# Optimization experiments

Hardware: AMD Instinct MI355X
Metric: run time of the kernel (lower is better)

The kernel has to match this reference:

```python
import jax, jax.numpy as jnp
import numpy as np
from jax import lax

# Production-scale dims: batch, seq_len, tag_size (incl. START/STOP tags)
B, S, T = 512, 512, 64


def setup_inputs() -> dict:
    key = jax.random.key(0)
    k1, k2, k3, k4 = jax.random.split(key, 4)
    feats = jax.random.normal(k1, (B, S, T), dtype=jnp.float32)
    # prefix-contiguous mask (module assumes mask[:, 0] == 1 and length-style masks)
    lengths = jax.random.randint(k2, (B,), S // 2, S + 1)
    mask = jnp.arange(S)[None, :] < lengths[:, None]  # (B, S) bool
    tags = jax.random.randint(k3, (B, S), 0, T - 2)  # gold tags exclude START/STOP
    transitions = jax.random.normal(k4, (T, T), dtype=jnp.float32) * 0.1
    return {"feats": feats, "mask": mask, "tags": tags, "transitions": transitions}


def _crf_nll(feats, transitions, mask, tags):
    b, s, t = feats.shape
    START, STOP = t - 2, t - 1  # START_TAG = -2, STOP_TAG = -1

    # ---- forward (log partition), matches _calculate_PZ ----
    # partition init: scores[0][:, START, :] = feats[:,0,:] + transitions[START, :]
    init = feats[:, 0, :] + transitions[START][None, :]  # (b, t)

    feats_t = jnp.swapaxes(feats, 0, 1)  # (s, b, t)
    mask_t = jnp.swapaxes(mask, 0, 1)    # (s, b)

    def step(partition, inp):
        f_t, m_t = inp  # (b, t), (b,)
        # cur_values[b, from, to] = feats_t[b, to] + transitions[from, to] + partition[b, from]
        cur = partition[:, :, None] + transitions[None, :, :] + f_t[:, None, :]
        new_p = jax.nn.logsumexp(cur, axis=1)  # reduce over 'from' -> (b, t)
        partition = jnp.where(m_t[:, None], new_p, partition)
        return partition, None

    partition, _ = lax.scan(step, init, (feats_t[1:], mask_t[1:]))

    # final transition to STOP
    final = jax.nn.logsumexp(partition[:, :, None] + transitions[None, :, :], axis=1)
    forward_score = final[:, STOP].sum()

    # ---- gold score, matches _score_sentence ----
    prev = jnp.concatenate(
        [jnp.full((b, 1), START, dtype=tags.dtype), tags[:, :-1]], axis=1
    )  # (b, s): previous tag, START at position 0
    emit = jnp.take_along_axis(feats, tags[:, :, None], axis=2)[:, :, 0]  # (b, s)
    tg_energy = emit + transitions[prev, tags]  # (b, s)
    gold = jnp.where(mask, tg_energy, jnp.zeros((), feats.dtype)).sum()
    lengths = mask.sum(axis=1).astype(jnp.int32)  # (b,)
    end_ids = jnp.take_along_axis(tags, (lengths - 1)[:, None].astype(tags.dtype), axis=1)[:, 0]
    gold = gold + transitions[end_ids, STOP].sum()

    # average_batch = False
    return forward_score - gold


def reference(feats, mask, tags, transitions):
    return _crf_nll(feats, transitions, mask, tags)
```

## Files before the change

### kernel.cpp

```cpp
#include <hip/hip_runtime.h>

#define BB 512
#define SS 512
#define TT 64
#define START_TAG 62
#define STOP_TAG 63

#define LOG2E 1.4426950408889634f
#define LN2   0.6931471805599453f

typedef _Float16 h2 __attribute__((ext_vector_type(2)));
typedef _Float16 h8 __attribute__((ext_vector_type(8)));
typedef float    f4 __attribute__((ext_vector_type(4)));

__device__ __forceinline__ h2 pkrtz(float a, float b) {
    return __builtin_bit_cast(h2, __builtin_amdgcn_cvt_pkrtz(a, b));
}
__device__ __forceinline__ f4 MF(h8 a, h8 b, f4 c) {
    return __builtin_amdgcn_mfma_f32_16x16x32_f16(a, b, c, 0, 0, 0);
}

__global__ void __launch_bounds__(192) crf_main(
    const float* __restrict__ feats, const int* __restrict__ mask,
    const int* __restrict__ tags, const float* __restrict__ trans,
    float* __restrict__ out)
{
    const int b    = blockIdx.x;
    const int tid  = threadIdx.x;
    const int wv   = tid >> 6;
    const int lane = tid & 63;

    const float* frow = feats + (size_t)b * SS * TT;
    const int*   mrow = mask + b * SS;

    __shared__ __align__(16) _Float16 febuf[2][8][TT];
    __shared__ __align__(16) float xbuf[TT];
    __shared__ __align__(16) float ybuf[TT];
    __shared__ int ks_sh;

    int cnt = 0;
    #pragma unroll
    for (int s = lane; s < SS; s += 64) cnt += (mrow[s] != 0);
    #pragma unroll
    for (int off = 32; off; off >>= 1) cnt += __shfl_xor(cnt, off);
    const int len = cnt;
    const int h   = len >> 1;

    float offs = 0.f;
    int   ksum = 0;

    if (wv < 2) {
        const bool isF = (wv == 0);
        const int g  = lane >> 4;
        const int cg = lane & 15;
        const int to_base = 16 * (cg >> 2) + (cg & 3);
        const int nstep = isF ? h : (len - h - 2);
        const int base  = isF ? 1 : (len - 2);
        const int dir   = isF ? 1 : -1;
        _Float16 (*febw)[TT] = febuf[wv];

        h8 A[4][2];
        #pragma unroll
        for (int tt = 0; tt < 4; ++tt)
            #pragma unroll
            for (int kc = 0; kc < 2; ++kc)
                #pragma unroll
                for (int j = 0; j < 8; ++j) {
                    const int kt = 16 * g + 8 * kc + j;
                    const int ot = to_base + 4 * tt;
                    const int ix = isF ? (kt * TT + ot) : (ot * TT + kt);
                    A[tt][kc][j] =
                        (_Float16)__builtin_amdgcn_exp2f(trans[ix] * LOG2E);
                }

        h8 B0, B1;
        if (isF) {
            offs = frow[0] + trans[START_TAG * TT + 0];
            #pragma unroll
            for (int sl = 0; sl < 8; ++sl) {
                const int t0 = 16 * g + sl, t1 = t0 + 8;
                B0[sl] = (_Float16)__builtin_amdgcn_exp2f(
                    (frow[t0] + trans[START_TAG * TT + t0] - offs) * LOG2E);
                B1[sl] = (_Float16)__builtin_amdgcn_exp2f(
                    (frow[t1] + trans[START_TAG * TT + t1] - offs) * LOG2E);
            }
        } else {
            const float* fl = frow + (size_t)(len - 1) * TT;
            #pragma unroll
            for (int sl = 0; sl < 8; ++sl) {
                const int t0 = 16 * g + sl, t1 = t0 + 8;
                B0[sl] = (_Float16)__builtin_amdgcn_exp2f(
                    (fl[t0] + trans[t0 * TT + STOP_TAG]) * LOG2E);
                B1[sl] = (_Float16)__builtin_amdgcn_exp2f(
                    (fl[t1] + trans[t1 * TT + STOP_TAG]) * LOG2E);
            }
        }

        auto rowOf = [&](int idx) {
            int r = base + dir * idx;
            return r < 0 ? 0 : (r > SS - 1 ? SS - 1 : r);
        };

        float fr[8];
        #pragma unroll
        for (int j = 0; j < 8; ++j)
            fr[j] = frow[(size_t)rowOf(j) * TT + lane];
        #pragma unroll
        for (int j = 0; j < 4; ++j)
            febw[rowOf(j) & 7][lane] =
                (_Float16)__builtin_amdgcn_exp2f(fr[j] * LOG2E);

        const f4 Zz = {0.f, 0.f, 0.f, 0.f};
        auto STEP = [&](int row) {
            const _Float16* fb = &febw[row & 7][16 * g];
            const h8 feL = *(const h8*)(fb);
            const h8 feH = *(const h8*)(fb + 8);
            f4 d0 = MF(A[0][0], B0, Zz);
            f4 d1 = MF(A[1][0], B0, Zz);
            f4 d2 = MF(A[2][0], B0, Zz);
            f4 d3 = MF(A[3][0], B0, Zz);
            d0 = MF(A[0][1], B1, d0);
            d1 = MF(A[1][1], B1, d1);
            d2 = MF(A[2][1], B1, d2);
            d3 = MF(A[3][1], B1, d3);
            const int eb = (__builtin_amdgcn_readfirstlane(
                                __float_as_int(d0[0])) >> 23) & 0xff;
            ksum += eb - 127;
            const float sc = __int_as_float((254 - eb) << 23);
            const h2 p0 = pkrtz(d0[0] * sc, d0[1] * sc);
            const h2 p1 = pkrtz(d0[2] * sc, d0[3] * sc);
            const h2 p2 = pkrtz(d1[0] * sc, d1[1] * sc);
            const h2 p3 = pkrtz(d1[2] * sc, d1[3] * sc);
            const h2 p4 = pkrtz(d2[0] * sc, d2[1] * sc);
            const h2 p5 = pkrtz(d2[2] * sc, d2[3] * sc);
            const h2 p6 = pkrtz(d3[0] * sc, d3[1] * sc);
            const h2 p7 = pkrtz(d3[2] * sc, d3[3] * sc);
            const h2 q0 = p0 * __builtin_shufflevector(feL, feL, 0, 1);
            const h2 q1 = p1 * __builtin_shufflevector(feL, feL, 2, 3);
            const h2 q2 = p2 * __builtin_shufflevector(feL, feL, 4, 5);
            const h2 q3 = p3 * __builtin_shufflevector(feL, feL, 6, 7);
            const h2 q4 = p4 * __builtin_shufflevector(feH, feH, 0, 1);
            const h2 q5 = p5 * __builtin_shufflevector(feH, feH, 2, 3);
            const h2 q6 = p6 * __builtin_shufflevector(feH, feH, 4, 5);
            const h2 q7 = p7 * __builtin_shufflevector(feH, feH, 6, 7);
            B0 = __builtin_shufflevector(
                     __builtin_shufflevector(q0, q1, 0, 1, 2, 3),
                     __builtin_shufflevector(q2, q3, 0, 1, 2, 3),
                     0, 1, 2, 3, 4, 5, 6, 7);
            B1 = __builtin_shufflevector(
                     __builtin_shufflevector(q4, q5, 0, 1, 2, 3),
                     __builtin_shufflevector(q6, q7, 0, 1, 2, 3),
                     0, 1, 2, 3, 4, 5, 6, 7);
        };

        int i = 0;
        for (; i + 3 < nstep; i += 4) {
            const float n0 = frow[(size_t)rowOf(i + 8)  * TT + lane];
            const float n1 = frow[(size_t)rowOf(i + 9)  * TT + lane];
            const float n2 = frow[(size_t)rowOf(i + 10) * TT + lane];
            const float n3 = frow[(size_t)rowOf(i + 11) * TT + lane];
            febw[rowOf(i + 4) & 7][lane] =
                (_Float16)__builtin_amdgcn_exp2f(fr[4] * LOG2E);
            febw[rowOf(i + 5) & 7][lane] =
                (_Float16)__builtin_amdgcn_exp2f(fr[5] * LOG2E);
            febw[rowOf(i + 6) & 7][lane] =
                (_Float16)__builtin_amdgcn_exp2f(fr[6] * LOG2E);
            febw[rowOf(i + 7) & 7][lane] =
                (_Float16)__builtin_amdgcn_exp2f(fr[7] * LOG2E);

            STEP(rowOf(i)); STEP(rowOf(i + 1));
            STEP(rowOf(i + 2)); STEP(rowOf(i + 3));

            #pragma unroll
            for (int j = 0; j < 4; ++j) fr[j] = fr[j + 4];
            fr[4] = n0; fr[5] = n1; fr[6] = n2; fr[7] = n3;
        }

        const int rem = nstep - i;
        if (rem > 0) STEP(rowOf(i));
        if (rem > 1) STEP(rowOf(i + 1));
        if (rem > 2) STEP(rowOf(i + 2));

        if (isF) {
            f4 d0 = MF(A[0][0], B0, Zz);
            f4 d1 = MF(A[1][0], B0, Zz);
            f4 d2 = MF(A[2][0], B0, Zz);
            f4 d3 = MF(A[3][0], B0, Zz);
            d0 = MF(A[0][1], B1, d0);
            d1 = MF(A[1][1], B1, d1);
            d2 = MF(A[2][1], B1, d2);
            d3 = MF(A[3][1], B1, d3);
            const int eb = (__builtin_amdgcn_readfirstlane(
                                __float_as_int(d0[0])) >> 23) & 0xff;
            ksum += eb - 127;
            const float sc = __int_as_float((254 - eb) << 23);
            if (cg == 0) {
                #pragma unroll
                for (int r = 0; r < 4; ++r) {
                    xbuf[16 * g + 0 * 4 + r] = d0[r] * sc;
                    xbuf[16 * g + 1 * 4 + r] = d1[r] * sc;
                    xbuf[16 * g + 2 * 4 + r] = d2[r] * sc;
                    xbuf[16 * g + 3 * 4 + r] = d3[r] * sc;
                }
            }
        } else {
            if (cg == 0) {
                #pragma unroll
                for (int sl = 0; sl < 8; ++sl) {
                    ybuf[16 * g + sl]     = (float)B0[sl];
                    ybuf[16 * g + 8 + sl] = (float)B1[sl];
                }
            }
            if (lane == 0) ks_sh = ksum;
        }
    } else {
        const int* trow = tags + b * SS;
        float acc = 0.f;
        for (int s = lane; s < SS; s += 64) {
            if (mrow[s] != 0) {
                const int tag  = trow[s];
                const int prev = (s == 0) ? START_TAG : trow[s - 1];
                acc += frow[(size_t)s * TT + tag] + trans[prev * TT + tag];
            }
        }
        #pragma unroll
        for (int off = 32; off; off >>= 1) acc += __shfl_xor(acc, off);
        if (lane == 0) {
            const int end_id = trow[len - 1];
            atomicAdd(out, -(acc + trans[end_id * TT + STOP_TAG]));
        }
    }

    __syncthreads();

    if (wv == 0) {
        float z = xbuf[lane] * ybuf[lane];
        #pragma unroll
        for (int off = 32; off; off >>= 1) z += __shfl_xor(z, off);
        if (lane == 0)
            atomicAdd(out, offs + (float)(ksum + ks_sh) * LN2
                           + LN2 * __builtin_amdgcn_logf(z));
    }
}

extern "C" void kernel_launch(void* const* d_in, const int* in_sizes, int n_in,
                              void* d_out, int out_size, void* d_ws, size_t ws_size,
                              hipStream_t stream) {
    const float* feats = (const float*)d_in[0];
    const int*   mask  = (const int*)d_in[1];
    const int*   tags  = (const int*)d_in[2];
    const float* trans = (const float*)d_in[3];
    float* out = (float*)d_out;

    (void)hipMemsetAsync(out, 0, sizeof(float), stream);
    crf_main<<<BB, 192, 0, stream>>>(feats, mask, tags, trans, out);
}
```

Measured before the change: 165.9 us.

## Merge forward and backward CRF recursions into one wave with interleaved chains

The forward and backward log-partition recursions, previously run by two separate waves, now run in a single wave that alternates steps of the two independent MFMA chains. This is meant to hide MFMA and conversion latency by giving the scheduler two dependency chains to overlap. It also removes the shared-memory handoff and block barrier: the final dot product is reduced with shuffles inside the wave. The block shrinks to two waves with a waves-per-EU hint. The trade-off is doubled per-wave register pressure and serialized instruction issue for both chains in one wave.

```diff
diff --git a/kernel.cpp b/kernel.cpp
--- a/kernel.cpp
+++ b/kernel.cpp
@@ -20,23 +20,20 @@
     return __builtin_amdgcn_mfma_f32_16x16x32_f16(a, b, c, 0, 0, 0);
 }
 
-__global__ void __launch_bounds__(192) crf_main(
+__global__ void __launch_bounds__(128)
+__attribute__((amdgpu_waves_per_eu(1, 1))) crf_main(
     const float* __restrict__ feats, const int* __restrict__ mask,
     const int* __restrict__ tags, const float* __restrict__ trans,
     float* __restrict__ out)
 {
     const int b    = blockIdx.x;
     const int tid  = threadIdx.x;
-    const int wv   = tid >> 6;
     const int lane = tid & 63;
 
     const float* frow = feats + (size_t)b * SS * TT;
     const int*   mrow = mask + b * SS;
 
     __shared__ __align__(16) _Float16 febuf[2][8][TT];
-    __shared__ __align__(16) float xbuf[TT];
-    __shared__ __align__(16) float ybuf[TT];
-    __shared__ int ks_sh;
 
     int cnt = 0;
     #pragma unroll
@@ -46,20 +43,14 @@
     const int len = cnt;
     const int h   = len >> 1;
 
-    float offs = 0.f;
-    int   ksum = 0;
-
-    if (wv < 2) {
-        const bool isF = (wv == 0);
+    if (tid < 64) {
         const int g  = lane >> 4;
         const int cg = lane & 15;
         const int to_base = 16 * (cg >> 2) + (cg & 3);
-        const int nstep = isF ? h : (len - h - 2);
-        const int base  = isF ? 1 : (len - 2);
-        const int dir   = isF ? 1 : -1;
-        _Float16 (*febw)[TT] = febuf[wv];
-
-        h8 A[4][2];
+        const int nf = h;
+        const int nb = len - h - 2;
+
+        h8 Af[4][2], Ab[4][2];
         #pragma unroll
         for (int tt = 0; tt < 4; ++tt)
             #pragma unroll
@@ -68,51 +59,44 @@
                 for (int j = 0; j < 8; ++j) {
                     const int kt = 16 * g + 8 * kc + j;
                     const int ot = to_base + 4 * tt;
-                    const int ix = isF ? (kt * TT + ot) : (ot * TT + kt);
-                    A[tt][kc][j] =
-                        (_Float16)__builtin_amdgcn_exp2f(trans[ix] * LOG2E);
+                    Af[tt][kc][j] = (_Float16)__builtin_amdgcn_exp2f(
+                        trans[kt * TT + ot] * LOG2E);
+                    Ab[tt][kc][j] = (_Float16)__builtin_amdgcn_exp2f(
+                        trans[ot * TT + kt] * LOG2E);
                 }
 
-        h8 B0, B1;
-        if (isF) {
-            offs = frow[0] + trans[START_TAG * TT + 0];
-            #pragma unroll
-            for (int sl = 0; sl < 8; ++sl) {
-                const int t0 = 16 * g + sl, t1 = t0 + 8;
-                B0[sl] = (_Float16)__builtin_amdgcn_exp2f(
-                    (frow[t0] + trans[START_TAG * TT + t0] - offs) * LOG2E);
-                B1[sl] = (_Float16)__builtin_amdgcn_exp2f(
-                    (frow[t1] + trans[START_TAG * TT + t1] - offs) * LOG2E);
-            }
-        } else {
+        const float offs = frow[0] + trans[START_TAG * TT + 0];
+        h8 Bf0, Bf1, Bb0, Bb1;
+        {
             const float* fl = frow + (size_t)(len - 1) * TT;
             #pragma unroll
             for (int sl = 0; sl < 8; ++sl) {
                 const int t0 = 16 * g + sl, t1 = t0 + 8;
-                B0[sl] = (_Float16)__builtin_amdgcn_exp2f(
+                Bf0[sl] = (_Float16)__builtin_amdgcn_exp2f(
+                    (frow[t0] + trans[START_TAG * TT + t0] - offs) * LOG2E);
+                Bf1[sl] = (_Float16)__builtin_amdgcn_exp2f(
+                    (frow[t1] + trans[START_TAG * TT + t1] - offs) * LOG2E);
+                Bb0[sl] = (_Float16)__builtin_amdgcn_exp2f(
                     (fl[t0] + trans[t0 * TT + STOP_TAG]) * LOG2E);
-                B1[sl] = (_Float16)__builtin_amdgcn_exp2f(
+                Bb1[sl] = (_Float16)__builtin_amdgcn_exp2f(
                     (fl[t1] + trans[t1 * TT + STOP_TAG]) * LOG2E);
             }
         }
-
-        auto rowOf = [&](int idx) {
-            int r = base + dir * idx;
-            return r < 0 ? 0 : (r > SS - 1 ? SS - 1 : r);
-        };
-
-        float fr[8];
-        #pragma unroll
-        for (int j = 0; j < 8; ++j)
-            fr[j] = frow[(size_t)rowOf(j) * TT + lane];
-        #pragma unroll
-        for (int j = 0; j < 4; ++j)
-            febw[rowOf(j) & 7][lane] =
-                (_Float16)__builtin_amdgcn_exp2f(fr[j] * LOG2E);
+        int ksf = 0, ksb = 0;
+
+        #pragma unroll
+        for (int j = 0; j < 4; ++j) {
+            const int rF = 1 + j, rB = len - 2 - j;
+            febuf[0][rF & 7][lane] = (_Float16)__builtin_amdgcn_exp2f(
+                frow[(size_t)rF * TT + lane] * LOG2E);
+            febuf[1][rB & 7][lane] = (_Float16)__builtin_amdgcn_exp2f(
+                frow[(size_t)rB * TT + lane] * LOG2E);
+        }
 
         const f4 Zz = {0.f, 0.f, 0.f, 0.f};
-        auto STEP = [&](int row) {
-            const _Float16* fb = &febw[row & 7][16 * g];
+        auto STEP = [&](const h8 (&A)[4][2], h8& B0, h8& B1,
+                        int ring, int row, int& ks) {
+            const _Float16* fb = &febuf[ring][row & 7][16 * g];
             const h8 feL = *(const h8*)(fb);
             const h8 feH = *(const h8*)(fb + 8);
             f4 d0 = MF(A[0][0], B0, Zz);
@@ -125,7 +109,7 @@
             d3 = MF(A[3][1], B1, d3);
             const int eb = (__builtin_amdgcn_readfirstlane(
                                 __float_as_int(d0[0])) >> 23) & 0xff;
-            ksum += eb - 127;
+            ks += eb - 127;
             const float sc = __int_as_float((254 - eb) << 23);
             const h2 p0 = pkrtz(d0[0] * sc, d0[1] * sc);
             const h2 p1 = pkrtz(d0[2] * sc, d0[3] * sc);
@@ -154,65 +138,69 @@
         };
 
         int i = 0;
-        for (; i + 3 < nstep; i += 4) {
-            const float n0 = frow[(size_t)rowOf(i + 8)  * TT + lane];
-            const float n1 = frow[(size_t)rowOf(i + 9)  * TT + lane];
-            const float n2 = frow[(size_t)rowOf(i + 10) * TT + lane];
-            const float n3 = frow[(size_t)rowOf(i + 11) * TT + lane];
-            febw[rowOf(i + 4) & 7][lane] =
-                (_Float16)__builtin_amdgcn_exp2f(fr[4] * LOG2E);
-            febw[rowOf(i + 5) & 7][lane] =
-                (_Float16)__builtin_amdgcn_exp2f(fr[5] * LOG2E);
-            febw[rowOf(i + 6) & 7][lane] =
-                (_Float16)__builtin_amdgcn_exp2f(fr[6] * LOG2E);
-            febw[rowOf(i + 7) & 7][lane] =
-                (_Float16)__builtin_amdgcn_exp2f(fr[7] * LOG2E);
-
-            STEP(rowOf(i)); STEP(rowOf(i + 1));
-            STEP(rowOf(i + 2)); STEP(rowOf(i + 3));
-
+        for (; i + 3 < nb; i += 4) {
             #pragma unroll
-            for (int j = 0; j < 4; ++j) fr[j] = fr[j + 4];
-            fr[4] = n0; fr[5] = n1; fr[6] = n2; fr[7] = n3;
-        }
-
-        const int rem = nstep - i;
-        if (rem > 0) STEP(rowOf(i));
-        if (rem > 1) STEP(rowOf(i + 1));
-        if (rem > 2) STEP(rowOf(i + 2));
-
-        if (isF) {
-            f4 d0 = MF(A[0][0], B0, Zz);
-            f4 d1 = MF(A[1][0], B0, Zz);
-            f4 d2 = MF(A[2][0], B0, Zz);
-            f4 d3 = MF(A[3][0], B0, Zz);
-            d0 = MF(A[0][1], B1, d0);
-            d1 = MF(A[1][1], B1, d1);
-            d2 = MF(A[2][1], B1, d2);
-            d3 = MF(A[3][1], B1, d3);
-            const int eb = (__builtin_amdgcn_readfirstlane(
-                                __float_as_int(d0[0])) >> 23) & 0xff;
-            ksum += eb - 127;
-            const float sc = __int_as_float((254 - eb) << 23);
-            if (cg == 0) {
-                #pragma unroll
-                for (int r = 0; r < 4; ++r) {
-                    xbuf[16 * g + 0 * 4 + r] = d0[r] * sc;
-                    xbuf[16 * g + 1 * 4 + r] = d1[r] * sc;
-                    xbuf[16 * g + 2 * 4 + r] = d2[r] * sc;
-                    xbuf[16 * g + 3 * 4 + r] = d3[r] * sc;
-                }
+            for (int j = 4; j < 8; ++j) {
+                const int rF = 1 + i + j;
+                const int rB = len - 2 - i - j;
+                febuf[0][rF & 7][lane] = (_Float16)__builtin_amdgcn_exp2f(
+                    frow[(size_t)rF * TT + lane] * LOG2E);
+                febuf[1][rB & 7][lane] = (_Float16)__builtin_amdgcn_exp2f(
+                    frow[(size_t)rB * TT + lane] * LOG2E);
             }
-        } else {
-            if (cg == 0) {
-                #pragma unroll
-                for (int sl = 0; sl < 8; ++sl) {
-                    ybuf[16 * g + sl]     = (float)B0[sl];
-                    ybuf[16 * g + 8 + sl] = (float)B1[sl];
-                }
-            }
-            if (lane == 0) ks_sh = ksum;
-        }
+
+            STEP(Af, Bf0, Bf1, 0, 1 + i,           ksf);
+            STEP(Ab, Bb0, Bb1, 1, len - 2 - i,     ksb);
+            STEP(Af, Bf0, Bf1, 0, 1 + i + 1,       ksf);
+            STEP(Ab, Bb0, Bb1, 1, len - 2 - i - 1, ksb);
+            STEP(Af, Bf0, Bf1, 0, 1 + i + 2,       ksf);
+            STEP(Ab, Bb0, Bb1, 1, len - 2 - i - 2, ksb);
+            STEP(Af, Bf0, Bf1, 0, 1 + i + 3,       ksf);
+            STEP(Ab, Bb0, Bb1, 1, len - 2 - i - 3, ksb);
+        }
+
+        const int rem = nb - i;
+        if (rem > 0) { STEP(Af, Bf0, Bf1, 0, 1 + i,     ksf);
+                       STEP(Ab, Bb0, Bb1, 1, len - 2 - i,     ksb); }
+        if (rem > 1) { STEP(Af, Bf0, Bf1, 0, 1 + i + 1, ksf);
+                       STEP(Ab, Bb0, Bb1, 1, len - 2 - i - 1, ksb); }
+        if (rem > 2) { STEP(Af, Bf0, Bf1, 0, 1 + i + 2, ksf);
+                       STEP(Ab, Bb0, Bb1, 1, len - 2 - i - 2, ksb); }
+
+        for (int k = nb; k < nf; ++k) {
+            const int rF = 1 + k;
+            febuf[0][rF & 7][lane] = (_Float16)__builtin_amdgcn_exp2f(
+                frow[(size_t)rF * TT + lane] * LOG2E);
+            STEP(Af, Bf0, Bf1, 0, rF, ksf);
+        }
+
+        f4 d0 = MF(Af[0][0], Bf0, Zz);
+        f4 d1 = MF(Af[1][0], Bf0, Zz);
+        f4 d2 = MF(Af[2][0], Bf0, Zz);
+        f4 d3 = MF(Af[3][0], Bf0, Zz);
+        d0 = MF(Af[0][1], Bf1, d0);
+        d1 = MF(Af[1][1], Bf1, d1);
+        d2 = MF(Af[2][1], Bf1, d2);
+        d3 = MF(Af[3][1], Bf1, d3);
+        const int eb = (__builtin_amdgcn_readfirstlane(
+                            __float_as_int(d0[0])) >> 23) & 0xff;
+        ksf += eb - 127;
+        const float sc = __int_as_float((254 - eb) << 23);
+
+        float z = 0.f;
+        #pragma unroll
+        for (int r = 0; r < 4; ++r) {
+            z += (d0[r] * sc) * (float)Bb0[r];
+            z += (d1[r] * sc) * (float)Bb0[4 + r];
+            z += (d2[r] * sc) * (float)Bb1[r];
+            z += (d3[r] * sc) * (float)Bb1[4 + r];
+        }
+        z += __shfl_xor(z, 16);
+        z += __shfl_xor(z, 32);
+
+        if (lane == 0)
+            atomicAdd(out, offs + (float)(ksf + ksb) * LN2
+                           + LN2 * __builtin_amdgcn_logf(z));
     } else {
         const int* trow = tags + b * SS;
         float acc = 0.f;
@@ -230,17 +218,6 @@
             atomicAdd(out, -(acc + trans[end_id * TT + STOP_TAG]));
         }
     }
-
-    __syncthreads();
-
-    if (wv == 0) {
-        float z = xbuf[lane] * ybuf[lane];
-        #pragma unroll
-        for (int off = 32; off; off >>= 1) z += __shfl_xor(z, off);
-        if (lane == 0)
-            atomicAdd(out, offs + (float)(ksum + ks_sh) * LN2
-                           + LN2 * __builtin_amdgcn_logf(z));
-    }
 }
 
 extern "C" void kernel_launch(void* const* d_in, const int* in_sizes, int n_in,
@@ -253,5 +230,5 @@
     float* out = (float*)d_out;
 
     (void)hipMemsetAsync(out, 0, sizeof(float), stream);
-    crf_main<<<BB, 192, 0, stream>>>(feats, mask, tags, trans, out);
-}
+    crf_main<<<BB, 128, 0, stream>>>(feats, mask, tags, trans, out);
+}
```

New measurement: 193.7 us. 1.17x slower.

## Split forward and backward recursions into separate single-wave blocks joined via workspace

Applied to the files above, without the earlier changes.

Each batch row's forward and backward half-recursions now run in separate 64-thread blocks (2*BB blocks) instead of two waves of one 192-thread block. The gold-score work is split in half across the two blocks. Partial results go to global workspace, and the second block to finish, detected through an atomic counter, combines them. The aim is to spread the serial recurrences over more CUs and drop the block-level barrier, at the cost of an extra memset, global-memory handoff and fences.

```diff
diff --git a/kernel.cpp b/kernel.cpp
--- a/kernel.cpp
+++ b/kernel.cpp
@@ -20,23 +20,28 @@
     return __builtin_amdgcn_mfma_f32_16x16x32_f16(a, b, c, 0, 0, 0);
 }
 
-__global__ void __launch_bounds__(192) crf_main(
+#define WS_FLAG(ws)  ((int*)(ws))
+#define WS_V(ws)     ((float*)((char*)(ws) + 2048))
+#define WS_U(ws)     ((float*)((char*)(ws) + 2048 + 131072))
+#define WS_K(ws)     ((int*)((char*)(ws) + 2048 + 262144))
+
+__global__ void __launch_bounds__(64)
+__attribute__((amdgpu_waves_per_eu(1, 1))) crf_main(
     const float* __restrict__ feats, const int* __restrict__ mask,
     const int* __restrict__ tags, const float* __restrict__ trans,
-    float* __restrict__ out)
+    float* __restrict__ out, void* __restrict__ ws)
 {
-    const int b    = blockIdx.x;
-    const int tid  = threadIdx.x;
-    const int wv   = tid >> 6;
-    const int lane = tid & 63;
+    const int bid  = blockIdx.x;
+    const bool isF = (bid < BB);
+    const int b    = isF ? bid : (bid - BB);
+    const int lane = threadIdx.x & 63;
+    const int g    = lane >> 4;
+    const int cg   = lane & 15;
 
     const float* frow = feats + (size_t)b * SS * TT;
     const int*   mrow = mask + b * SS;
 
-    __shared__ __align__(16) _Float16 febuf[2][8][TT];
-    __shared__ __align__(16) float xbuf[TT];
-    __shared__ __align__(16) float ybuf[TT];
-    __shared__ int ks_sh;
+    __shared__ __align__(16) _Float16 febw[8][TT];
 
     int cnt = 0;
     #pragma unroll
@@ -46,177 +51,12 @@
     const int len = cnt;
     const int h   = len >> 1;
 
-    float offs = 0.f;
-    int   ksum = 0;
-
-    if (wv < 2) {
-        const bool isF = (wv == 0);
-        const int g  = lane >> 4;
-        const int cg = lane & 15;
-        const int to_base = 16 * (cg >> 2) + (cg & 3);
-        const int nstep = isF ? h : (len - h - 2);
-        const int base  = isF ? 1 : (len - 2);
-        const int dir   = isF ? 1 : -1;
-        _Float16 (*febw)[TT] = febuf[wv];
-
-        h8 A[4][2];
-        #pragma unroll
-        for (int tt = 0; tt < 4; ++tt)
-            #pragma unroll
-            for (int kc = 0; kc < 2; ++kc)
-                #pragma unroll
-                for (int j = 0; j < 8; ++j) {
-                    const int kt = 16 * g + 8 * kc + j;
-                    const int ot = to_base + 4 * tt;
-                    const int ix = isF ? (kt * TT + ot) : (ot * TT + kt);
-                    A[tt][kc][j] =
-                        (_Float16)__builtin_amdgcn_exp2f(trans[ix] * LOG2E);
-                }
-
-        h8 B0, B1;
-        if (isF) {
-            offs = frow[0] + trans[START_TAG * TT + 0];
-            #pragma unroll
-            for (int sl = 0; sl < 8; ++sl) {
-                const int t0 = 16 * g + sl, t1 = t0 + 8;
-                B0[sl] = (_Float16)__builtin_amdgcn_exp2f(
-                    (frow[t0] + trans[START_TAG * TT + t0] - offs) * LOG2E);
-                B1[sl] = (_Float16)__builtin_amdgcn_exp2f(
-                    (frow[t1] + trans[START_TAG * TT + t1] - offs) * LOG2E);
-            }
-        } else {
-            const float* fl = frow + (size_t)(len - 1) * TT;
-            #pragma unroll
-            for (int sl = 0; sl < 8; ++sl) {
-                const int t0 = 16 * g + sl, t1 = t0 + 8;
-                B0[sl] = (_Float16)__builtin_amdgcn_exp2f(
-                    (fl[t0] + trans[t0 * TT + STOP_TAG]) * LOG2E);
-                B1[sl] = (_Float16)__builtin_amdgcn_exp2f(
-                    (fl[t1] + trans[t1 * TT + STOP_TAG]) * LOG2E);
-            }
-        }
-
-        auto rowOf = [&](int idx) {
-            int r = base + dir * idx;
-            return r < 0 ? 0 : (r > SS - 1 ? SS - 1 : r);
-        };
-
-        float fr[8];
-        #pragma unroll
-        for (int j = 0; j < 8; ++j)
-            fr[j] = frow[(size_t)rowOf(j) * TT + lane];
-        #pragma unroll
-        for (int j = 0; j < 4; ++j)
-            febw[rowOf(j) & 7][lane] =
-                (_Float16)__builtin_amdgcn_exp2f(fr[j] * LOG2E);
-
-        const f4 Zz = {0.f, 0.f, 0.f, 0.f};
-        auto STEP = [&](int row) {
-            const _Float16* fb = &febw[row & 7][16 * g];
-            const h8 feL = *(const h8*)(fb);
-            const h8 feH = *(const h8*)(fb + 8);
-            f4 d0 = MF(A[0][0], B0, Zz);
-            f4 d1 = MF(A[1][0], B0, Zz);
-            f4 d2 = MF(A[2][0], B0, Zz);
-            f4 d3 = MF(A[3][0], B0, Zz);
-            d0 = MF(A[0][1], B1, d0);
-            d1 = MF(A[1][1], B1, d1);
-            d2 = MF(A[2][1], B1, d2);
-            d3 = MF(A[3][1], B1, d3);
-            const int eb = (__builtin_amdgcn_readfirstlane(
-                                __float_as_int(d0[0])) >> 23) & 0xff;
-            ksum += eb - 127;
-            const float sc = __int_as_float((254 - eb) << 23);
-            const h2 p0 = pkrtz(d0[0] * sc, d0[1] * sc);
-            const h2 p1 = pkrtz(d0[2] * sc, d0[3] * sc);
-            const h2 p2 = pkrtz(d1[0] * sc, d1[1] * sc);
-            const h2 p3 = pkrtz(d1[2] * sc, d1[3] * sc);
-            const h2 p4 = pkrtz(d2[0] * sc, d2[1] * sc);
-            const h2 p5 = pkrtz(d2[2] * sc, d2[3] * sc);
-            const h2 p6 = pkrtz(d3[0] * sc, d3[1] * sc);
-            const h2 p7 = pkrtz(d3[2] * sc, d3[3] * sc);
-            const h2 q0 = p0 * __builtin_shufflevector(feL, feL, 0, 1);
-            const h2 q1 = p1 * __builtin_shufflevector(feL, feL, 2, 3);
-            const h2 q2 = p2 * __builtin_shufflevector(feL, feL, 4, 5);
-            const h2 q3 = p3 * __builtin_shufflevector(feL, feL, 6, 7);
-            const h2 q4 = p4 * __builtin_shufflevector(feH, feH, 0, 1);
-            const h2 q5 = p5 * __builtin_shufflevector(feH, feH, 2, 3);
-            const h2 q6 = p6 * __builtin_shufflevector(feH, feH, 4, 5);
-            const h2 q7 = p7 * __builtin_shufflevector(feH, feH, 6, 7);
-            B0 = __builtin_shufflevector(
-                     __builtin_shufflevector(q0, q1, 0, 1, 2, 3),
-                     __builtin_shufflevector(q2, q3, 0, 1, 2, 3),
-                     0, 1, 2, 3, 4, 5, 6, 7);
-            B1 = __builtin_shufflevector(
-                     __builtin_shufflevector(q4, q5, 0, 1, 2, 3),
-                     __builtin_shufflevector(q6, q7, 0, 1, 2, 3),
-                     0, 1, 2, 3, 4, 5, 6, 7);
-        };
-
-        int i = 0;
-        for (; i + 3 < nstep; i += 4) {
-            const float n0 = frow[(size_t)rowOf(i + 8)  * TT + lane];
-            const float n1 = frow[(size_t)rowOf(i + 9)  * TT + lane];
-            const float n2 = frow[(size_t)rowOf(i + 10) * TT + lane];
-            const float n3 = frow[(size_t)rowOf(i + 11) * TT + lane];
-            febw[rowOf(i + 4) & 7][lane] =
-                (_Float16)__builtin_amdgcn_exp2f(fr[4] * LOG2E);
-            febw[rowOf(i + 5) & 7][lane] =
-                (_Float16)__builtin_amdgcn_exp2f(fr[5] * LOG2E);
-            febw[rowOf(i + 6) & 7][lane] =
-                (_Float16)__builtin_amdgcn_exp2f(fr[6] * LOG2E);
-            febw[rowOf(i + 7) & 7][lane] =
-                (_Float16)__builtin_amdgcn_exp2f(fr[7] * LOG2E);
-
-            STEP(rowOf(i)); STEP(rowOf(i + 1));
-            STEP(rowOf(i + 2)); STEP(rowOf(i + 3));
-
-            #pragma unroll
-            for (int j = 0; j < 4; ++j) fr[j] = fr[j + 4];
-            fr[4] = n0; fr[5] = n1; fr[6] = n2; fr[7] = n3;
-        }
-
-        const int rem = nstep - i;
-        if (rem > 0) STEP(rowOf(i));
-        if (rem > 1) STEP(rowOf(i + 1));
-        if (rem > 2) STEP(rowOf(i + 2));
-
-        if (isF) {
-            f4 d0 = MF(A[0][0], B0, Zz);
-            f4 d1 = MF(A[1][0], B0, Zz);
-            f4 d2 = MF(A[2][0], B0, Zz);
-            f4 d3 = MF(A[3][0], B0, Zz);
-            d0 = MF(A[0][1], B1, d0);
-            d1 = MF(A[1][1], B1, d1);
-            d2 = MF(A[2][1], B1, d2);
-            d3 = MF(A[3][1], B1, d3);
-            const int eb = (__builtin_amdgcn_readfirstlane(
-                                __float_as_int(d0[0])) >> 23) & 0xff;
-            ksum += eb - 127;
-            const float sc = __int_as_float((254 - eb) << 23);
-            if (cg == 0) {
-                #pragma unroll
-                for (int r = 0; r < 4; ++r) {
-                    xbuf[16 * g + 0 * 4 + r] = d0[r] * sc;
-                    xbuf[16 * g + 1 * 4 + r] = d1[r] * sc;
-                    xbuf[16 * g + 2 * 4 + r] = d2[r] * sc;
-                    xbuf[16 * g + 3 * 4 + r] = d3[r] * sc;
-                }
-            }
-        } else {
-            if (cg == 0) {
-                #pragma unroll
-                for (int sl = 0; sl < 8; ++sl) {
-                    ybuf[16 * g + sl]     = (float)B0[sl];
-                    ybuf[16 * g + 8 + sl] = (float)B1[sl];
-                }
-            }
-            if (lane == 0) ks_sh = ksum;
-        }
-    } else {
+    {
         const int* trow = tags + b * SS;
         float acc = 0.f;
-        for (int s = lane; s < SS; s += 64) {
+        const int s0 = isF ? lane : (256 + lane);
+        const int s1 = isF ? 256 : 512;
+        for (int s = s0; s < s1; s += 64) {
             if (mrow[s] != 0) {
                 const int tag  = trow[s];
                 const int prev = (s == 0) ? START_TAG : trow[s - 1];
@@ -226,20 +66,195 @@
         #pragma unroll
         for (int off = 32; off; off >>= 1) acc += __shfl_xor(acc, off);
         if (lane == 0) {
-            const int end_id = trow[len - 1];
-            atomicAdd(out, -(acc + trans[end_id * TT + STOP_TAG]));
-        }
-    }
-
-    __syncthreads();
-
-    if (wv == 0) {
-        float z = xbuf[lane] * ybuf[lane];
+            float extra = 0.f;
+            if (!isF) extra = trans[trow[len - 1] * TT + STOP_TAG];
+            atomicAdd(out, -(acc + extra));
+        }
+    }
+
+    const int to_base = 16 * (cg >> 2) + (cg & 3);
+    const int nstep = isF ? h : (len - h - 2);
+    const int base  = isF ? 1 : (len - 2);
+    const int dir   = isF ? 1 : -1;
+
+    h8 A[4][2];
+    #pragma unroll
+    for (int tt = 0; tt < 4; ++tt)
+        #pragma unroll
+        for (int kc = 0; kc < 2; ++kc)
+            #pragma unroll
+            for (int j = 0; j < 8; ++j) {
+                const int kt = 16 * g + 8 * kc + j;
+                const int ot = to_base + 4 * tt;
+                const int ix = isF ? (kt * TT + ot) : (ot * TT + kt);
+                A[tt][kc][j] =
+                    (_Float16)__builtin_amdgcn_exp2f(trans[ix] * LOG2E);
+            }
+
+    h8 B0, B1;
+    if (isF) {
+        const float offs = frow[0] + trans[START_TAG * TT + 0];
+        #pragma unroll
+        for (int sl = 0; sl < 8; ++sl) {
+            const int t0 = 16 * g + sl, t1 = t0 + 8;
+            B0[sl] = (_Float16)__builtin_amdgcn_exp2f(
+                (frow[t0] + trans[START_TAG * TT + t0] - offs) * LOG2E);
+            B1[sl] = (_Float16)__builtin_amdgcn_exp2f(
+                (frow[t1] + trans[START_TAG * TT + t1] - offs) * LOG2E);
+        }
+    } else {
+        const float* fl = frow + (size_t)(len - 1) * TT;
+        #pragma unroll
+        for (int sl = 0; sl < 8; ++sl) {
+            const int t0 = 16 * g + sl, t1 = t0 + 8;
+            B0[sl] = (_Float16)__builtin_amdgcn_exp2f(
+                (fl[t0] + trans[t0 * TT + STOP_TAG]) * LOG2E);
+            B1[sl] = (_Float16)__builtin_amdgcn_exp2f(
+                (fl[t1] + trans[t1 * TT + STOP_TAG]) * LOG2E);
+        }
+    }
+    int ksum = 0;
+
+    auto rowOf = [&](int idx) {
+        int r = base + dir * idx;
+        return r < 0 ? 0 : (r > SS - 1 ? SS - 1 : r);
+    };
+
+    float fr[8];
+    #pragma unroll
+    for (int j = 0; j < 8; ++j)
+        fr[j] = frow[(size_t)rowOf(j) * TT + lane];
+    #pragma unroll
+    for (int j = 0; j < 4; ++j)
+        febw[rowOf(j) & 7][lane] =
+            (_Float16)__builtin_amdgcn_exp2f(fr[j] * LOG2E);
+
+    const f4 Zz = {0.f, 0.f, 0.f, 0.f};
+    auto STEP = [&](int row) {
+        const _Float16* fb = &febw[row & 7][16 * g];
+        const h8 feL = *(const h8*)(fb);
+        const h8 feH = *(const h8*)(fb + 8);
+        f4 d0 = MF(A[0][0], B0, Zz);
+        f4 d1 = MF(A[1][0], B0, Zz);
+        f4 d2 = MF(A[2][0], B0, Zz);
+        f4 d3 = MF(A[3][0], B0, Zz);
+        d0 = MF(A[0][1], B1, d0);
+        d1 = MF(A[1][1], B1, d1);
+        d2 = MF(A[2][1], B1, d2);
+        d3 = MF(A[3][1], B1, d3);
+        const int eb = (__builtin_amdgcn_readfirstlane(
+                            __float_as_int(d0[0])) >> 23) & 0xff;
+        ksum += eb - 127;
+        const float sc = __int_as_float((254 - eb) << 23);
+        const h2 p0 = pkrtz(d0[0] * sc, d0[1] * sc);
+        const h2 p1 = pkrtz(d0[2] * sc, d0[3] * sc);
+        const h2 p2 = pkrtz(d1[0] * sc, d1[1] * sc);
+        const h2 p3 = pkrtz(d1[2] * sc, d1[3] * sc);
+        const h2 p4 = pkrtz(d2[0] * sc, d2[1] * sc);
+        const h2 p5 = pkrtz(d2[2] * sc, d2[3] * sc);
+        const h2 p6 = pkrtz(d3[0] * sc, d3[1] * sc);
+        const h2 p7 = pkrtz(d3[2] * sc, d3[3] * sc);
+        const h2 q0 = p0 * __builtin_shufflevector(feL, feL, 0, 1);
+        const h2 q1 = p1 * __builtin_shufflevector(feL, feL, 2, 3);
+        const h2 q2 = p2 * __builtin_shufflevector(feL, feL, 4, 5);
+        const h2 q3 = p3 * __builtin_shufflevector(feL, feL, 6, 7);
+        const h2 q4 = p4 * __builtin_shufflevector(feH, feH, 0, 1);
+        const h2 q5 = p5 * __builtin_shufflevector(feH, feH, 2, 3);
+        const h2 q6 = p6 * __builtin_shufflevector(feH, feH, 4, 5);
+        const h2 q7 = p7 * __builtin_shufflevector(feH, feH, 6, 7);
+        B0 = __builtin_shufflevector(
+                 __builtin_shufflevector(q0, q1, 0, 1, 2, 3),
+                 __builtin_shufflevector(q2, q3, 0, 1, 2, 3),
+                 0, 1, 2, 3, 4, 5, 6, 7);
+        B1 = __builtin_shufflevector(
+                 __builtin_shufflevector(q4, q5, 0, 1, 2, 3),
+                 __builtin_shufflevector(q6, q7, 0, 1, 2, 3),
+                 0, 1, 2, 3, 4, 5, 6, 7);
+    };
+
+    int i = 0;
+    for (; i + 3 < nstep; i += 4) {
+        const float n0 = frow[(size_t)rowOf(i + 8)  * TT + lane];
+        const float n1 = frow[(size_t)rowOf(i + 9)  * TT + lane];
+        const float n2 = frow[(size_t)rowOf(i + 10) * TT + lane];
+        const float n3 = frow[(size_t)rowOf(i + 11) * TT + lane];
+        febw[rowOf(i + 4) & 7][lane] =
+            (_Float16)__builtin_amdgcn_exp2f(fr[4] * LOG2E);
+        febw[rowOf(i + 5) & 7][lane] =
+            (_Float16)__builtin_amdgcn_exp2f(fr[5] * LOG2E);
+        febw[rowOf(i + 6) & 7][lane] =
+            (_Float16)__builtin_amdgcn_exp2f(fr[6] * LOG2E);
+        febw[rowOf(i + 7) & 7][lane] =
+            (_Float16)__builtin_amdgcn_exp2f(fr[7] * LOG2E);
+
+        STEP(rowOf(i)); STEP(rowOf(i + 1));
+        STEP(rowOf(i + 2)); STEP(rowOf(i + 3));
+
+        #pragma unroll
+        for (int j = 0; j < 4; ++j) fr[j] = fr[j + 4];
+        fr[4] = n0; fr[5] = n1; fr[6] = n2; fr[7] = n3;
+    }
+
+    const int rem = nstep - i;
+    if (rem > 0) STEP(rowOf(i));
+    if (rem > 1) STEP(rowOf(i + 1));
+    if (rem > 2) STEP(rowOf(i + 2));
+
+    float* Vws = WS_V(ws) + b * TT;
+    float* Uws = WS_U(ws) + b * TT;
+    int*   Kws = WS_K(ws) + b * 2;
+
+    if (isF) {
+        f4 d0 = MF(A[0][0], B0, Zz);
+        f4 d1 = MF(A[1][0], B0, Zz);
+        f4 d2 = MF(A[2][0], B0, Zz);
+        f4 d3 = MF(A[3][0], B0, Zz);
+        d0 = MF(A[0][1], B1, d0);
+        d1 = MF(A[1][1], B1, d1);
+        d2 = MF(A[2][1], B1, d2);
+        d3 = MF(A[3][1], B1, d3);
+        const int eb = (__builtin_amdgcn_readfirstlane(
+                            __float_as_int(d0[0])) >> 23) & 0xff;
+        ksum += eb - 127;
+        const float sc = __int_as_float((254 - eb) << 23);
+        if (cg == 0) {
+            #pragma unroll
+            for (int r = 0; r < 4; ++r) {
+                Vws[16 * g + 0 * 4 + r] = d0[r] * sc;
+                Vws[16 * g + 1 * 4 + r] = d1[r] * sc;
+                Vws[16 * g + 2 * 4 + r] = d2[r] * sc;
+                Vws[16 * g + 3 * 4 + r] = d3[r] * sc;
+            }
+        }
+        if (lane == 0) Kws[0] = ksum;
+    } else {
+        if (cg == 0) {
+            #pragma unroll
+            for (int sl = 0; sl < 8; ++sl) {
+                Uws[16 * g + sl]     = (float)B0[sl];
+                Uws[16 * g + 8 + sl] = (float)B1[sl];
+            }
+        }
+        if (lane == 0) Kws[1] = ksum;
+    }
+
+    __threadfence();
+    int old = 0;
+    if (lane == 0) old = atomicAdd(&WS_FLAG(ws)[b], 1);
+    old = __shfl(old, 0);
+    if (old == 1) {
+        __threadfence();
+        const volatile float* Vv = Vws;
+        const volatile float* Uv = Uws;
+        const volatile int*   Kv = Kws;
+        float z = Vv[lane] * Uv[lane];
         #pragma unroll
         for (int off = 32; off; off >>= 1) z += __shfl_xor(z, off);
-        if (lane == 0)
-            atomicAdd(out, offs + (float)(ksum + ks_sh) * LN2
+        if (lane == 0) {
+            const float offs = frow[0] + trans[START_TAG * TT + 0];
+            atomicAdd(out, offs + (float)(Kv[0] + Kv[1]) * LN2
                            + LN2 * __builtin_amdgcn_logf(z));
+        }
     }
 }
 
@@ -253,5 +268,6 @@
     float* out = (float*)d_out;
 
     (void)hipMemsetAsync(out, 0, sizeof(float), stream);
-    crf_main<<<BB, 192, 0, stream>>>(feats, mask, tags, trans, out);
-}
+    (void)hipMemsetAsync(d_ws, 0, 2048, stream);
+    crf_main<<<2 * BB, 64, 0, stream>>>(feats, mask, tags, trans, out, d_ws);
+}
```

New measurement: 197.6 us. 1.19x slower.
